# Optimization experiments

Hardware: AMD Instinct MI355X
Metric: run time of the kernel (lower is better)

## Reference

```python
import jax, jax.numpy as jnp
import numpy as np

N_SRC = 200000
N_EDGES = 1280000
N_SEG = 100000
D = 64


def setup_inputs() -> dict:
    key = jax.random.key(0)
    k1, k2, k3 = jax.random.split(key, 3)
    values = jax.random.normal(k1, (N_SRC, D), dtype=jnp.float32)
    gather_idx = jax.random.randint(k2, (N_EDGES,), 0, N_SRC, dtype=jnp.int64)
    segment_ids = jnp.sort(jax.random.randint(k3, (N_EDGES,), 0, N_SEG, dtype=jnp.int64))
    return {
        "values": values,
        "gather_idx": gather_idx,
        "segment_ids": segment_ids,
        "num_segments": N_SEG,
    }


def reference(values, gather_idx, segment_ids, num_segments):
    # AGG_GATHER: indexed gather of input values  -> [E, D]
    gathered = values[gather_idx]
    # AGG_SCATTER_REDUCE: scatter_mean over ragged segments (sorted ids)
    sums = jax.ops.segment_sum(gathered, segment_ids, num_segments=num_segments,
                               indices_are_sorted=True)
    counts = jax.ops.segment_sum(jnp.ones((gathered.shape[0],), dtype=values.dtype),
                                 segment_ids, num_segments=num_segments,
                                 indices_are_sorted=True)
    # mean = sum / count (guard empty segments)
    return sums / jnp.maximum(counts, 1.0)[:, None]
```

## Files before the change

kernel.cpp:

```cpp
#include <hip/hip_runtime.h>


#define D 64

__global__ __launch_bounds__(256) void seg_starts_kernel(
    const int* __restrict__ segment_ids,
    int*       __restrict__ starts,
    int n_edges, int n_seg)
{
    const int e       = blockIdx.x * blockDim.x + threadIdx.x;
    const bool active = (e < n_edges);
    const int ec      = active ? e : (n_edges - 1);
    const int s       = segment_ids[ec];
    const int lane    = threadIdx.x & 63;
    int sprev         = __shfl_up(s, 1, 64);
    if (lane == 0) sprev = (ec == 0) ? -1 : segment_ids[ec - 1];
    if (active) {
        for (int t = sprev + 1; t <= s; ++t) starts[t] = e;
        if (e == n_edges - 1) {
            for (int t = s + 1; t <= n_seg; ++t) starts[t] = n_edges;
        }
    }
}

__global__ __launch_bounds__(256) void seg_mean_kernel(
    const float* __restrict__ values,
    const int*   __restrict__ gather_idx,
    const int*   __restrict__ starts,
    float*       __restrict__ out,
    int n_seg)
{
    const int wave = (blockIdx.x * blockDim.x + threadIdx.x) >> 6;
    const int lane = threadIdx.x & 63;
    const int s0 = wave << 1;
    if (s0 >= n_seg) return;
    const int s1 = s0 + 1;
    const bool has1 = (s1 < n_seg);

    const int sub = lane >> 4;
    const int cg  = lane & 15;

    const int st0 = starts[s0];
    const int en0 = starts[s0 + 1];
    const int st1 = en0;
    const int en1 = has1 ? starts[s1 + 1] : en0;

    float4 acc0 = make_float4(0.f, 0.f, 0.f, 0.f);
    float4 acc1 = make_float4(0.f, 0.f, 0.f, 0.f);

    int b0 = st0, b1 = st1;
    while (b0 < en0 || b1 < en1) {
        const int ea0 = b0 + 0  + sub, ea1 = b0 + 4  + sub;
        const int ea2 = b0 + 8  + sub, ea3 = b0 + 12 + sub;
        const int eb0 = b1 + 0  + sub, eb1 = b1 + 4  + sub;
        const int eb2 = b1 + 8  + sub, eb3 = b1 + 12 + sub;
        const bool ma0 = ea0 < en0, ma1 = ea1 < en0, ma2 = ea2 < en0, ma3 = ea3 < en0;
        const bool mb0 = eb0 < en1, mb1 = eb1 < en1, mb2 = eb2 < en1, mb3 = eb3 < en1;
        const int ia0 = gather_idx[ma0 ? ea0 : 0];
        const int ia1 = gather_idx[ma1 ? ea1 : 0];
        const int ia2 = gather_idx[ma2 ? ea2 : 0];
        const int ia3 = gather_idx[ma3 ? ea3 : 0];
        const int ib0 = gather_idx[mb0 ? eb0 : 0];
        const int ib1 = gather_idx[mb1 ? eb1 : 0];
        const int ib2 = gather_idx[mb2 ? eb2 : 0];
        const int ib3 = gather_idx[mb3 ? eb3 : 0];
        const float4 va0 = *(const float4*)(values + ((long long)ia0 << 6) + (cg << 2));
        const float4 va1 = *(const float4*)(values + ((long long)ia1 << 6) + (cg << 2));
        const float4 va2 = *(const float4*)(values + ((long long)ia2 << 6) + (cg << 2));
        const float4 va3 = *(const float4*)(values + ((long long)ia3 << 6) + (cg << 2));
        const float4 vb0 = *(const float4*)(values + ((long long)ib0 << 6) + (cg << 2));
        const float4 vb1 = *(const float4*)(values + ((long long)ib1 << 6) + (cg << 2));
        const float4 vb2 = *(const float4*)(values + ((long long)ib2 << 6) + (cg << 2));
        const float4 vb3 = *(const float4*)(values + ((long long)ib3 << 6) + (cg << 2));
        acc0.x += ma0 ? va0.x : 0.f; acc0.y += ma0 ? va0.y : 0.f;
        acc0.z += ma0 ? va0.z : 0.f; acc0.w += ma0 ? va0.w : 0.f;
        acc0.x += ma1 ? va1.x : 0.f; acc0.y += ma1 ? va1.y : 0.f;
        acc0.z += ma1 ? va1.z : 0.f; acc0.w += ma1 ? va1.w : 0.f;
        acc0.x += ma2 ? va2.x : 0.f; acc0.y += ma2 ? va2.y : 0.f;
        acc0.z += ma2 ? va2.z : 0.f; acc0.w += ma2 ? va2.w : 0.f;
        acc0.x += ma3 ? va3.x : 0.f; acc0.y += ma3 ? va3.y : 0.f;
        acc0.z += ma3 ? va3.z : 0.f; acc0.w += ma3 ? va3.w : 0.f;
        acc1.x += mb0 ? vb0.x : 0.f; acc1.y += mb0 ? vb0.y : 0.f;
        acc1.z += mb0 ? vb0.z : 0.f; acc1.w += mb0 ? vb0.w : 0.f;
        acc1.x += mb1 ? vb1.x : 0.f; acc1.y += mb1 ? vb1.y : 0.f;
        acc1.z += mb1 ? vb1.z : 0.f; acc1.w += mb1 ? vb1.w : 0.f;
        acc1.x += mb2 ? vb2.x : 0.f; acc1.y += mb2 ? vb2.y : 0.f;
        acc1.z += mb2 ? vb2.z : 0.f; acc1.w += mb2 ? vb2.w : 0.f;
        acc1.x += mb3 ? vb3.x : 0.f; acc1.y += mb3 ? vb3.y : 0.f;
        acc1.z += mb3 ? vb3.z : 0.f; acc1.w += mb3 ? vb3.w : 0.f;
        b0 += 16; b1 += 16;
    }

    acc0.x += __shfl_xor(acc0.x, 16, 64); acc0.y += __shfl_xor(acc0.y, 16, 64);
    acc0.z += __shfl_xor(acc0.z, 16, 64); acc0.w += __shfl_xor(acc0.w, 16, 64);
    acc0.x += __shfl_xor(acc0.x, 32, 64); acc0.y += __shfl_xor(acc0.y, 32, 64);
    acc0.z += __shfl_xor(acc0.z, 32, 64); acc0.w += __shfl_xor(acc0.w, 32, 64);
    acc1.x += __shfl_xor(acc1.x, 16, 64); acc1.y += __shfl_xor(acc1.y, 16, 64);
    acc1.z += __shfl_xor(acc1.z, 16, 64); acc1.w += __shfl_xor(acc1.w, 16, 64);
    acc1.x += __shfl_xor(acc1.x, 32, 64); acc1.y += __shfl_xor(acc1.y, 32, 64);
    acc1.z += __shfl_xor(acc1.z, 32, 64); acc1.w += __shfl_xor(acc1.w, 32, 64);

    const int c0 = en0 - st0;
    const int c1 = en1 - st1;
    const float inv0 = (c0 > 0) ? (1.0f / (float)c0) : 1.0f;
    const float inv1 = (c1 > 0) ? (1.0f / (float)c1) : 1.0f;

    if (sub == 0 || (sub == 1 && has1)) {
        float4 r;
        if (sub == 0) {
            r.x = acc0.x * inv0; r.y = acc0.y * inv0;
            r.z = acc0.z * inv0; r.w = acc0.w * inv0;
        } else {
            r.x = acc1.x * inv1; r.y = acc1.y * inv1;
            r.z = acc1.z * inv1; r.w = acc1.w * inv1;
        }
        const int s = s0 + sub;
        *(float4*)(out + ((long long)s << 6) + (cg << 2)) = r;
    }
}

__global__ __launch_bounds__(256) void seg_mean_bsearch_kernel(
    const float* __restrict__ values,
    const int*   __restrict__ gather_idx,
    const int*   __restrict__ segment_ids,
    float*       __restrict__ out,
    int n_edges, int n_seg)
{
    const int wave = (blockIdx.x * blockDim.x + threadIdx.x) >> 6;
    const int lane = threadIdx.x & 63;
    if (wave >= n_seg) return;
    const int s = wave;
    int lo = 0, hi = n_edges;
    while (lo < hi) { int mid = (lo + hi) >> 1; if (segment_ids[mid] < s) lo = mid + 1; else hi = mid; }
    const int start = lo;
    hi = n_edges;
    while (lo < hi) { int mid = (lo + hi) >> 1; if (segment_ids[mid] < s + 1) lo = mid + 1; else hi = mid; }
    const int end = lo;
    float sum = 0.0f;
    for (int e = start; e < end; ++e) sum += values[((long long)gather_idx[e] << 6) + lane];
    const int count = end - start;
    const float inv = (count > 0) ? (1.0f / (float)count) : 1.0f;
    out[((long long)s << 6) + lane] = sum * inv;
}

extern "C" void kernel_launch(void* const* d_in, const int* in_sizes, int n_in,
                              void* d_out, int out_size, void* d_ws, size_t ws_size,
                              hipStream_t stream) {
    const float* values      = (const float*)d_in[0];
    const int*   gather_idx  = (const int*)d_in[1];
    const int*   segment_ids = (const int*)d_in[2];
    float* out = (float*)d_out;

    const int n_edges = in_sizes[1];
    const int n_seg   = out_size / D;

    const size_t starts_bytes = (size_t)(n_seg + 1) * sizeof(int);
    if (ws_size >= starts_bytes) {
        int* starts = (int*)d_ws;
        {
            const int threads = 256;
            const int blocks  = (n_edges + threads - 1) / threads;
            seg_starts_kernel<<<blocks, threads, 0, stream>>>(
                segment_ids, starts, n_edges, n_seg);
        }
        {
            const int n_waves = (n_seg + 1) >> 1;
            const int threads = 256;
            const int blocks  = (n_waves * 64 + threads - 1) / threads;
            seg_mean_kernel<<<blocks, threads, 0, stream>>>(
                values, gather_idx, starts, out, n_seg);
        }
    } else {
        const int threads = 256;
        const int blocks  = (n_seg * 64 + threads - 1) / threads;
        seg_mean_bsearch_kernel<<<blocks, threads, 0, stream>>>(
            values, gather_idx, segment_ids, out, n_edges, n_seg);
    }
}
```

Before: 137.7 us.

## Convert values table to bf16 before gather to halve gather bytes

Adds a pre-pass that converts the fp32 values table to bf16 (round-to-nearest-even) in workspace, with a zero pad row, and the segment-mean kernel then gathers 8-byte bf16 chunks instead of 16-byte fp32 chunks and widens them to fp32 for accumulation. Masked lanes now point at the zero pad row instead of reloading index 0. The aim is to cut random-gather memory traffic, but it adds a full conversion pass over the 51 MB table every call and lowers input precision, which may fail tolerance checks.

Result: faster. 133.4 us (median of 2 runs) (-3.1%).

```diff
diff --git a/kernel.cpp b/kernel.cpp
--- a/kernel.cpp
+++ b/kernel.cpp
@@ -2,6 +2,34 @@
 
 
 #define D 64
+
+__global__ __launch_bounds__(256) void convert_bf16_kernel(
+    const float* __restrict__ src,
+    unsigned short* __restrict__ dst,
+    int n, int n_padded)
+{
+    const int i = (blockIdx.x * blockDim.x + threadIdx.x) * 8;
+    if (i >= n_padded) return;
+    float4 a = make_float4(0.f, 0.f, 0.f, 0.f);
+    float4 b = make_float4(0.f, 0.f, 0.f, 0.f);
+    if (i < n) {
+        a = *(const float4*)(src + i);
+        b = *(const float4*)(src + i + 4);
+    }
+    #define PACK_BF16(x, y) ({                                         \
+        unsigned ux = __float_as_uint(x);                              \
+        unsigned uy = __float_as_uint(y);                              \
+        ux = (ux + 0x7FFFu + ((ux >> 16) & 1u)) >> 16;                 \
+        uy = (uy + 0x7FFFu + ((uy >> 16) & 1u)) >> 16;                 \
+        ux | (uy << 16); })
+    uint4 o;
+    o.x = PACK_BF16(a.x, a.y);
+    o.y = PACK_BF16(a.z, a.w);
+    o.z = PACK_BF16(b.x, b.y);
+    o.w = PACK_BF16(b.z, b.w);
+    #undef PACK_BF16
+    *(uint4*)(dst + i) = o;
+}
 
 __global__ __launch_bounds__(256) void seg_starts_kernel(
     const int* __restrict__ segment_ids,
@@ -23,12 +51,12 @@
     }
 }
 
-__global__ __launch_bounds__(256) void seg_mean_kernel(
-    const float* __restrict__ values,
+__global__ __launch_bounds__(256) void seg_mean_bf16_kernel(
+    const unsigned short* __restrict__ vals16,
     const int*   __restrict__ gather_idx,
     const int*   __restrict__ starts,
     float*       __restrict__ out,
-    int n_seg)
+    int n_seg, int n_src)
 {
     const int wave = (blockIdx.x * blockDim.x + threadIdx.x) >> 6;
     const int lane = threadIdx.x & 63;
@@ -44,6 +72,8 @@
     const int en0 = starts[s0 + 1];
     const int st1 = en0;
     const int en1 = has1 ? starts[s1 + 1] : en0;
+
+    const uint2* __restrict__ rows = (const uint2*)vals16;
 
     float4 acc0 = make_float4(0.f, 0.f, 0.f, 0.f);
     float4 acc1 = make_float4(0.f, 0.f, 0.f, 0.f);
@@ -56,38 +86,30 @@
         const int eb2 = b1 + 8  + sub, eb3 = b1 + 12 + sub;
         const bool ma0 = ea0 < en0, ma1 = ea1 < en0, ma2 = ea2 < en0, ma3 = ea3 < en0;
         const bool mb0 = eb0 < en1, mb1 = eb1 < en1, mb2 = eb2 < en1, mb3 = eb3 < en1;
-        const int ia0 = gather_idx[ma0 ? ea0 : 0];
-        const int ia1 = gather_idx[ma1 ? ea1 : 0];
-        const int ia2 = gather_idx[ma2 ? ea2 : 0];
-        const int ia3 = gather_idx[ma3 ? ea3 : 0];
-        const int ib0 = gather_idx[mb0 ? eb0 : 0];
-        const int ib1 = gather_idx[mb1 ? eb1 : 0];
-        const int ib2 = gather_idx[mb2 ? eb2 : 0];
-        const int ib3 = gather_idx[mb3 ? eb3 : 0];
-        const float4 va0 = *(const float4*)(values + ((long long)ia0 << 6) + (cg << 2));
-        const float4 va1 = *(const float4*)(values + ((long long)ia1 << 6) + (cg << 2));
-        const float4 va2 = *(const float4*)(values + ((long long)ia2 << 6) + (cg << 2));
-        const float4 va3 = *(const float4*)(values + ((long long)ia3 << 6) + (cg << 2));
-        const float4 vb0 = *(const float4*)(values + ((long long)ib0 << 6) + (cg << 2));
-        const float4 vb1 = *(const float4*)(values + ((long long)ib1 << 6) + (cg << 2));
-        const float4 vb2 = *(const float4*)(values + ((long long)ib2 << 6) + (cg << 2));
-        const float4 vb3 = *(const float4*)(values + ((long long)ib3 << 6) + (cg << 2));
-        acc0.x += ma0 ? va0.x : 0.f; acc0.y += ma0 ? va0.y : 0.f;
-        acc0.z += ma0 ? va0.z : 0.f; acc0.w += ma0 ? va0.w : 0.f;
-        acc0.x += ma1 ? va1.x : 0.f; acc0.y += ma1 ? va1.y : 0.f;
-        acc0.z += ma1 ? va1.z : 0.f; acc0.w += ma1 ? va1.w : 0.f;
-        acc0.x += ma2 ? va2.x : 0.f; acc0.y += ma2 ? va2.y : 0.f;
-        acc0.z += ma2 ? va2.z : 0.f; acc0.w += ma2 ? va2.w : 0.f;
-        acc0.x += ma3 ? va3.x : 0.f; acc0.y += ma3 ? va3.y : 0.f;
-        acc0.z += ma3 ? va3.z : 0.f; acc0.w += ma3 ? va3.w : 0.f;
-        acc1.x += mb0 ? vb0.x : 0.f; acc1.y += mb0 ? vb0.y : 0.f;
-        acc1.z += mb0 ? vb0.z : 0.f; acc1.w += mb0 ? vb0.w : 0.f;
-        acc1.x += mb1 ? vb1.x : 0.f; acc1.y += mb1 ? vb1.y : 0.f;
-        acc1.z += mb1 ? vb1.z : 0.f; acc1.w += mb1 ? vb1.w : 0.f;
-        acc1.x += mb2 ? vb2.x : 0.f; acc1.y += mb2 ? vb2.y : 0.f;
-        acc1.z += mb2 ? vb2.z : 0.f; acc1.w += mb2 ? vb2.w : 0.f;
-        acc1.x += mb3 ? vb3.x : 0.f; acc1.y += mb3 ? vb3.y : 0.f;
-        acc1.z += mb3 ? vb3.z : 0.f; acc1.w += mb3 ? vb3.w : 0.f;
+        const int ia0 = ma0 ? gather_idx[ea0] : n_src;
+        const int ia1 = ma1 ? gather_idx[ea1] : n_src;
+        const int ia2 = ma2 ? gather_idx[ea2] : n_src;
+        const int ia3 = ma3 ? gather_idx[ea3] : n_src;
+        const int ib0 = mb0 ? gather_idx[eb0] : n_src;
+        const int ib1 = mb1 ? gather_idx[eb1] : n_src;
+        const int ib2 = mb2 ? gather_idx[eb2] : n_src;
+        const int ib3 = mb3 ? gather_idx[eb3] : n_src;
+        const uint2 va0 = rows[((long long)ia0 << 4) + cg];
+        const uint2 va1 = rows[((long long)ia1 << 4) + cg];
+        const uint2 va2 = rows[((long long)ia2 << 4) + cg];
+        const uint2 va3 = rows[((long long)ia3 << 4) + cg];
+        const uint2 vb0 = rows[((long long)ib0 << 4) + cg];
+        const uint2 vb1 = rows[((long long)ib1 << 4) + cg];
+        const uint2 vb2 = rows[((long long)ib2 << 4) + cg];
+        const uint2 vb3 = rows[((long long)ib3 << 4) + cg];
+        #define ACC(A, V)                                              \
+            A.x += __uint_as_float((V).x << 16);                       \
+            A.y += __uint_as_float((V).x & 0xFFFF0000u);               \
+            A.z += __uint_as_float((V).y << 16);                       \
+            A.w += __uint_as_float((V).y & 0xFFFF0000u);
+        ACC(acc0, va0) ACC(acc0, va1) ACC(acc0, va2) ACC(acc0, va3)
+        ACC(acc1, vb0) ACC(acc1, vb1) ACC(acc1, vb2) ACC(acc1, vb3)
+        #undef ACC
         b0 += 16; b1 += 16;
     }
 
@@ -151,24 +173,36 @@
     const int*   segment_ids = (const int*)d_in[2];
     float* out = (float*)d_out;
 
-    const int n_edges = in_sizes[1];
-    const int n_seg   = out_size / D;
-
-    const size_t starts_bytes = (size_t)(n_seg + 1) * sizeof(int);
-    if (ws_size >= starts_bytes) {
-        int* starts = (int*)d_ws;
+    const int n_values = in_sizes[0];
+    const int n_edges  = in_sizes[1];
+    const int n_seg    = out_size / D;
+    const int n_src    = n_values / D;
+
+    const int    n_padded    = n_values + D;
+    const size_t table_bytes = (size_t)n_padded * sizeof(unsigned short);
+    const size_t starts_off  = (table_bytes + 15) & ~(size_t)15;
+    const size_t need        = starts_off + (size_t)(n_seg + 1) * sizeof(int);
+
+    if (ws_size >= need) {
+        unsigned short* vals16 = (unsigned short*)d_ws;
+        int* starts = (int*)((char*)d_ws + starts_off);
         {
             const int threads = 256;
-            const int blocks  = (n_edges + threads - 1) / threads;
-            seg_starts_kernel<<<blocks, threads, 0, stream>>>(
+            const int n_thr   = n_padded / 8;
+            convert_bf16_kernel<<<(n_thr + threads - 1) / threads, threads, 0, stream>>>(
+                values, vals16, n_values, n_padded);
+        }
+        {
+            const int threads = 256;
+            seg_starts_kernel<<<(n_edges + threads - 1) / threads, threads, 0, stream>>>(
                 segment_ids, starts, n_edges, n_seg);
         }
         {
             const int n_waves = (n_seg + 1) >> 1;
             const int threads = 256;
             const int blocks  = (n_waves * 64 + threads - 1) / threads;
-            seg_mean_kernel<<<blocks, threads, 0, stream>>>(
-                values, gather_idx, starts, out, n_seg);
+            seg_mean_bf16_kernel<<<blocks, threads, 0, stream>>>(
+                vals16, gather_idx, starts, out, n_seg, n_src);
         }
     } else {
         const int threads = 256;
```
